# Performance work log

Measured on AMD Instinct MI355X. Metric: run time of the kernel, lower is better.

The kernel has to match this reference:

```python
import jax, jax.numpy as jnp
import numpy as np

D = 1024

def setup_inputs() -> dict:
    key = jax.random.key(0)
    ks = jax.random.split(key, 7)
    s = 1.0 / np.sqrt(D)  # torch Linear default init scale (uniform bound)
    x = jax.random.normal(ks[0], (4, 2048, D), dtype=jnp.float32)
    Wq = jax.random.uniform(ks[1], (D, D), jnp.float32, -s, s)
    Wk = jax.random.uniform(ks[2], (D, D), jnp.float32, -s, s)
    Wv = jax.random.uniform(ks[3], (D, D), jnp.float32, -s, s)
    bq = jax.random.uniform(ks[4], (D,), jnp.float32, -s, s)
    bk = jax.random.uniform(ks[5], (D,), jnp.float32, -s, s)
    bv = jax.random.uniform(ks[6], (D,), jnp.float32, -s, s)
    return {"x": x, "Wq": Wq, "bq": bq, "Wk": Wk, "bk": bk, "Wv": Wv, "bv": bv}

def reference(x, Wq, bq, Wk, bk, Wv, bv):
    # Linear layers: y = x @ W^T + b (weights stored torch-style [out, in])
    Q = jnp.einsum('bsd,ed->bse', x, Wq) + bq
    K = jnp.einsum('bsd,ed->bse', x, Wk) + bk
    V = jnp.einsum('bsd,ed->bse', x, Wv) + bv
    scale = jnp.sqrt(jnp.asarray(Q.shape[-1], Q.dtype))
    scores = jnp.einsum('bqd,bkd->bqk', Q, K) / scale  # [B, S, S]
    probs = jax.nn.softmax(scores, axis=-1)
    return jnp.einsum('bqk,bkd->bqd', probs, V)
```

## Files before the change

kernel.cpp:

```cpp
#include <hip/hip_runtime.h>


typedef __bf16 bf16x8 __attribute__((ext_vector_type(8)));
typedef float f32x4 __attribute__((ext_vector_type(4)));
typedef unsigned short u16;

__device__ __forceinline__ u16 f2b(float f) {
  union { float f; unsigned u; } a; a.f = f;
  unsigned r = a.u + 0x7fffu + ((a.u >> 16) & 1u);
  return (u16)(r >> 16);
}

__global__ __launch_bounds__(256) void cast_all_kernel(const float* __restrict__ x,
                                                       const float* __restrict__ Wq,
                                                       const float* __restrict__ Wk,
                                                       const float* __restrict__ Wv,
                                                       u16* __restrict__ xb,
                                                       u16* __restrict__ Wb) {
  int b = blockIdx.x;
  if (b < 8192) {
    const int i = b * 256 + threadIdx.x;
    float4 v = reinterpret_cast<const float4*>(x)[i];
    reinterpret_cast<ushort4*>(xb)[i] =
        make_ushort4(f2b(v.x), f2b(v.y), f2b(v.z), f2b(v.w));
  } else {
    b -= 8192;
    const int w = b >> 10;
    const float* src = (w == 0) ? Wq : (w == 1) ? Wk : Wv;
    const int i = (b & 1023) * 256 + threadIdx.x;
    float4 v = reinterpret_cast<const float4*>(src)[i];
    reinterpret_cast<ushort4*>(Wb + (size_t)w * 1048576)[i] =
        make_ushort4(f2b(v.x), f2b(v.y), f2b(v.z), f2b(v.w));
  }
}

template <int GEOM, int NT>
__device__ __forceinline__ void core2(const char* __restrict__ Ab,
                                      const char* __restrict__ Bb, int lda, int ldb,
                                      char* smem, f32x4* acc) {
  constexpr int LDSBUF = GEOM ? 49152 : 65536;
  constexpr int BOFF = GEOM ? 16384 : 32768;
  constexpr int AHALF = GEOM ? 8192 : 16384;
  constexpr int NA = GEOM ? 4 : 8;
  const int tid = threadIdx.x;
  const int wave = tid >> 6, lane = tid & 63;
  const int wr = wave >> 2, wc = wave & 3;
  const int fr = lane & 15, fg = lane >> 4;
  const int rd = (fr * 64 + fg * 16) ^ (((fr >> 3) & 1) << 5);
  const int li = (lane * 16) ^ ((lane >> 5) << 5);
  const int sr = li >> 6, sc2 = li & 63;

  auto STAGE = [&](int kt, int s) {
    char* base = smem + (kt & 1) * LDSBUF;
    const int colOff = kt * 128 + s * 64 + sc2;
    char* ldsA = base + s * AHALF;
    __builtin_amdgcn_global_load_lds(
        (const __attribute__((address_space(1))) void*)(Ab + (size_t)(wave * 16 + sr) * lda + colOff),
        (__attribute__((address_space(3))) void*)(ldsA + wave * 1024), 16, 0, 0);
    if constexpr (GEOM == 0)
      __builtin_amdgcn_global_load_lds(
          (const __attribute__((address_space(1))) void*)(Ab + (size_t)((8 + wave) * 16 + sr) * lda + colOff),
          (__attribute__((address_space(3))) void*)(ldsA + 8192 + wave * 1024), 16, 0, 0);
    char* ldsB = base + BOFF + s * 16384;
    __builtin_amdgcn_global_load_lds(
        (const __attribute__((address_space(1))) void*)(Bb + (size_t)(wave * 16 + sr) * ldb + colOff),
        (__attribute__((address_space(3))) void*)(ldsB + wave * 1024), 16, 0, 0);
    __builtin_amdgcn_global_load_lds(
        (const __attribute__((address_space(1))) void*)(Bb + (size_t)((8 + wave) * 16 + sr) * ldb + colOff),
        (__attribute__((address_space(3))) void*)(ldsB + 8192 + wave * 1024), 16, 0, 0);
  };

  STAGE(0, 0);
  STAGE(0, 1);
  if constexpr (GEOM == 0) asm volatile("s_waitcnt vmcnt(4)" ::: "memory");
  else asm volatile("s_waitcnt vmcnt(3)" ::: "memory");
  __builtin_amdgcn_s_barrier();
  __builtin_amdgcn_sched_barrier(0);

  for (int kt = 0; kt < NT; ++kt) {
    const char* bufA = smem + (kt & 1) * LDSBUF;
    const char* bufB = bufA + BOFF;
#pragma unroll
    for (int s = 0; s < 2; ++s) {
      bf16x8 afr[NA], bfr[4];
#pragma unroll
      for (int m = 0; m < NA; ++m)
        afr[m] = *reinterpret_cast<const bf16x8*>(bufA + s * AHALF + (wr * NA + m) * 1024 + rd);
#pragma unroll
      for (int n = 0; n < 4; ++n)
        bfr[n] = *reinterpret_cast<const bf16x8*>(bufB + s * 16384 + (wc * 4 + n) * 1024 + rd);
      if (kt + 1 < NT) STAGE(kt + 1, s);
      __builtin_amdgcn_s_barrier();
      __builtin_amdgcn_sched_barrier(0);
      __builtin_amdgcn_s_setprio(1);
#pragma unroll
      for (int m = 0; m < NA; ++m)
#pragma unroll
        for (int n = 0; n < 4; ++n)
          acc[m * 4 + n] = __builtin_amdgcn_mfma_f32_16x16x32_bf16(
              afr[m], bfr[n], acc[m * 4 + n], 0, 0, 0);
      __builtin_amdgcn_s_setprio(0);
      if (kt < NT - 1) {
        if constexpr (GEOM == 0) asm volatile("s_waitcnt vmcnt(4)" ::: "memory");
        else asm volatile("s_waitcnt vmcnt(3)" ::: "memory");
      } else if (s == 0) {
        asm volatile("s_waitcnt vmcnt(0)" ::: "memory");
      }
      __builtin_amdgcn_s_barrier();
      __builtin_amdgcn_sched_barrier(0);
    }
  }
}

__global__ __launch_bounds__(512, 2) void proj8_kernel(
    const u16* __restrict__ A, const u16* __restrict__ Bm,
    const float* __restrict__ bq, const float* __restrict__ bk,
    const float* __restrict__ bvv, u16* __restrict__ QK, u16* __restrict__ Vt) {
  extern __shared__ char smem[];
  const int tileM = blockIdx.x * 128, tileN = blockIdx.y * 256;
  f32x4 acc[16] = {};
  core2<1, 16>((const char*)A + (size_t)tileM * 2048,
               (const char*)Bm + (size_t)tileN * 2048, 2048, 2048, smem, acc);
  const int tid = threadIdx.x;
  const int wave = tid >> 6, lane = tid & 63;
  const int wr = wave >> 2, wc = wave & 3, fr = lane & 15, fg = lane >> 4;
  const int w = blockIdx.y >> 2;
  const float* bias = (w == 0) ? bq : (w == 1) ? bk : bvv;
  if (w < 2) {
    u16* O = QK + (size_t)w * 8388608;
#pragma unroll
    for (int mi = 0; mi < 4; ++mi) {
      const int r0 = tileM + wr * 64 + mi * 16 + fg * 4;
#pragma unroll
      for (int n = 0; n < 4; ++n) {
        const int cw = (tileN + wc * 64 + n * 16 + fr) & 1023;
        const float bi = bias[cw];
#pragma unroll
        for (int jj = 0; jj < 4; ++jj)
          O[(size_t)(r0 + jj) * 1024 + cw] = f2b(acc[mi * 4 + n][jj] + bi);
      }
    }
  } else {
#pragma unroll
    for (int mi = 0; mi < 4; ++mi) {
      const int r0 = tileM + wr * 64 + mi * 16 + fg * 4;
      const int b = r0 >> 11, s0 = r0 & 2047;
#pragma unroll
      for (int n = 0; n < 4; ++n) {
        const int cw = (tileN + wc * 64 + n * 16 + fr) & 1023;
        const float bi = bias[cw];
        ushort4 u = make_ushort4(f2b(acc[mi * 4 + n][0] + bi), f2b(acc[mi * 4 + n][1] + bi),
                                 f2b(acc[mi * 4 + n][2] + bi), f2b(acc[mi * 4 + n][3] + bi));
        *reinterpret_cast<ushort4*>(&Vt[(size_t)b * 2097152 + (size_t)cw * 2048 + s0]) = u;
      }
    }
  }
}

__global__ __launch_bounds__(512, 2) void sc8_kernel(const u16* __restrict__ Qb,
                                                     const u16* __restrict__ Kb,
                                                     u16* __restrict__ P,
                                                     float* __restrict__ rowpart) {
  extern __shared__ char smem[];
  const int z = blockIdx.z;
  const int tileM = blockIdx.x * 256, tileN = blockIdx.y * 256;
  f32x4 acc[32] = {};
  core2<0, 16>((const char*)Qb + (size_t)z * 4194304 + (size_t)tileM * 2048,
               (const char*)Kb + (size_t)z * 4194304 + (size_t)tileN * 2048, 2048, 2048,
               smem, acc);
  const int tid = threadIdx.x;
  const int wave = tid >> 6, lane = tid & 63;
  const int wr = wave >> 2, wc = wave & 3, fr = lane & 15, fg = lane >> 4;
  float* rs = (float*)smem;
  u16* Po = P + (size_t)z * 4194304 + (size_t)tileM * 2048 + tileN;
#pragma unroll
  for (int mi = 0; mi < 8; ++mi) {
#pragma unroll
    for (int jj = 0; jj < 4; ++jj) {
      const int rl = wr * 128 + mi * 16 + fg * 4 + jj;
      float part = 0.f;
#pragma unroll
      for (int n = 0; n < 4; ++n) {
        float e = __expf(acc[mi * 4 + n][jj] * 0.03125f);
        part += e;
        Po[(size_t)rl * 2048 + wc * 64 + n * 16 + fr] = f2b(e);
      }
      part += __shfl_xor(part, 1);
      part += __shfl_xor(part, 2);
      part += __shfl_xor(part, 4);
      part += __shfl_xor(part, 8);
      if (fr == 0) rs[wc * 256 + rl] = part;
    }
  }
  __syncthreads();
  if (tid < 256) {
    float s = rs[tid] + rs[256 + tid] + rs[512 + tid] + rs[768 + tid];
    rowpart[(size_t)blockIdx.y * 8192 + z * 2048 + tileM + tid] = s;
  }
}

__global__ __launch_bounds__(512, 2) void pv8_kernel(const u16* __restrict__ P,
                                                     const u16* __restrict__ Vt,
                                                     const float* __restrict__ rowpart,
                                                     float* __restrict__ out) {
  extern __shared__ char smem[];
  const int z = blockIdx.z;
  const int tileM = blockIdx.x * 128, tileN = blockIdx.y * 256;
  float* rinv = (float*)(smem + 98304);
  const int tid = threadIdx.x;
  if (tid < 128) {
    float s = 0.f;
#pragma unroll
    for (int t = 0; t < 8; ++t) s += rowpart[t * 8192 + z * 2048 + tileM + tid];
    rinv[tid] = 1.0f / s;
  }
  __builtin_amdgcn_sched_barrier(0);
  f32x4 acc[16] = {};
  core2<1, 32>((const char*)P + (size_t)z * 8388608 + (size_t)tileM * 4096,
               (const char*)Vt + (size_t)z * 4194304 + (size_t)tileN * 4096, 4096, 4096,
               smem, acc);
  const int wave = tid >> 6, lane = tid & 63;
  const int wr = wave >> 2, wc = wave & 3, fr = lane & 15, fg = lane >> 4;
  float* O = out + (size_t)z * 2097152;
#pragma unroll
  for (int mi = 0; mi < 4; ++mi) {
#pragma unroll
    for (int jj = 0; jj < 4; ++jj) {
      const int r = wr * 64 + mi * 16 + fg * 4 + jj;
      const float inv = rinv[r];
#pragma unroll
      for (int n = 0; n < 4; ++n)
        O[(size_t)(tileM + r) * 1024 + tileN + wc * 64 + n * 16 + fr] =
            acc[mi * 4 + n][jj] * inv;
    }
  }
}

extern "C" void kernel_launch(void* const* d_in, const int* in_sizes, int n_in,
                              void* d_out, int out_size, void* d_ws, size_t ws_size,
                              hipStream_t stream) {
  if (ws_size < ((size_t)72 << 20)) return;
  const float* x = (const float*)d_in[0];
  const float* Wq = (const float*)d_in[1];
  const float* bq = (const float*)d_in[2];
  const float* Wk = (const float*)d_in[3];
  const float* bk = (const float*)d_in[4];
  const float* Wv = (const float*)d_in[5];
  const float* bv = (const float*)d_in[6];
  char* ws = (char*)d_ws;
  u16* xb = (u16*)(ws);
  u16* Pb = (u16*)(ws);
  u16* Qb = (u16*)(ws + ((size_t)16 << 20));
  u16* Kb = (u16*)(ws + ((size_t)32 << 20));
  u16* Vt = (u16*)(ws + ((size_t)48 << 20));
  u16* Wb = (u16*)(ws + ((size_t)64 << 20));
  float* rowpart = (float*)(ws + ((size_t)70 << 20));
  float* out = (float*)d_out;

  (void)hipFuncSetAttribute((const void*)proj8_kernel,
                            hipFuncAttributeMaxDynamicSharedMemorySize, 98304);
  (void)hipFuncSetAttribute((const void*)sc8_kernel,
                            hipFuncAttributeMaxDynamicSharedMemorySize, 131072);
  (void)hipFuncSetAttribute((const void*)pv8_kernel,
                            hipFuncAttributeMaxDynamicSharedMemorySize, 98816);

  cast_all_kernel<<<11264, 256, 0, stream>>>(x, Wq, Wk, Wv, xb, Wb);

  proj8_kernel<<<dim3(64, 12), 512, 98304, stream>>>(xb, Wb, bq, bk, bv, Qb, Vt);

  sc8_kernel<<<dim3(8, 8, 4), 512, 131072, stream>>>(Qb, Kb, Pb, rowpart);
  pv8_kernel<<<dim3(16, 4, 4), 512, 98816, stream>>>(Pb, Vt, rowpart, out);
}
```

Before: 155.5 us.

## Software-pipeline GEMM core: prefetch LDS fragments before MFMAs and deepen staging

Restructures the shared GEMM main loop used by all three matmul kernels. It issues one extra half-stage of global-to-LDS loads ahead, and loads the next sub-step's A/B fragments from LDS into a second register set while the MFMAs of the current sub-step run. Both changes aim to hide LDS read latency and global load latency behind MFMA work. In exchange it uses more registers for the double fragment buffers, which could add spills or lower occupancy, and its waitcnt and barrier choreography is more intricate and easier to get wrong.

```diff
diff --git a/kernel.cpp b/kernel.cpp
--- a/kernel.cpp
+++ b/kernel.cpp
@@ -34,10 +34,12 @@
   }
 }
 
+#define VMCNT(n) asm volatile("s_waitcnt vmcnt(" #n ")" ::: "memory")
+
 template <int GEOM, int NT>
-__device__ __forceinline__ void core2(const char* __restrict__ Ab,
-                                      const char* __restrict__ Bb, int lda, int ldb,
-                                      char* smem, f32x4* acc) {
+__device__ __forceinline__ void core2p(const char* __restrict__ Ab,
+                                       const char* __restrict__ Bb, int lda, int ldb,
+                                       char* smem, f32x4* acc) {
   constexpr int LDSBUF = GEOM ? 49152 : 65536;
   constexpr int BOFF = GEOM ? 16384 : 32768;
   constexpr int AHALF = GEOM ? 8192 : 16384;
@@ -69,46 +71,67 @@
         (const __attribute__((address_space(1))) void*)(Bb + (size_t)((8 + wave) * 16 + sr) * ldb + colOff),
         (__attribute__((address_space(3))) void*)(ldsB + 8192 + wave * 1024), 16, 0, 0);
   };
+  auto RD_A = [&](const char* buf, int s, bf16x8* a) {
+#pragma unroll
+    for (int m = 0; m < NA; ++m)
+      a[m] = *reinterpret_cast<const bf16x8*>(buf + s * AHALF + (wr * NA + m) * 1024 + rd);
+  };
+  auto RD_B = [&](const char* buf, int s, bf16x8* b) {
+#pragma unroll
+    for (int n = 0; n < 4; ++n)
+      b[n] = *reinterpret_cast<const bf16x8*>(buf + BOFF + s * 16384 + (wc * 4 + n) * 1024 + rd);
+  };
+  auto MFMA = [&](bf16x8* a, bf16x8* b) {
+    __builtin_amdgcn_s_setprio(1);
+#pragma unroll
+    for (int m = 0; m < NA; ++m)
+#pragma unroll
+      for (int n = 0; n < 4; ++n)
+        acc[m * 4 + n] = __builtin_amdgcn_mfma_f32_16x16x32_bf16(a[m], b[n], acc[m * 4 + n], 0, 0, 0);
+    __builtin_amdgcn_s_setprio(0);
+  };
 
   STAGE(0, 0);
   STAGE(0, 1);
-  if constexpr (GEOM == 0) asm volatile("s_waitcnt vmcnt(4)" ::: "memory");
-  else asm volatile("s_waitcnt vmcnt(3)" ::: "memory");
+  STAGE(1, 0);
+  if constexpr (GEOM == 0) VMCNT(8); else VMCNT(6);
   __builtin_amdgcn_s_barrier();
   __builtin_amdgcn_sched_barrier(0);
 
+  bf16x8 a0[NA], a1[NA], b0[4], b1[4];
+  RD_A(smem, 0, a0);
+  if constexpr (GEOM == 1) RD_B(smem, 0, b0);
+
   for (int kt = 0; kt < NT; ++kt) {
-    const char* bufA = smem + (kt & 1) * LDSBUF;
-    const char* bufB = bufA + BOFF;
-#pragma unroll
-    for (int s = 0; s < 2; ++s) {
-      bf16x8 afr[NA], bfr[4];
-#pragma unroll
-      for (int m = 0; m < NA; ++m)
-        afr[m] = *reinterpret_cast<const bf16x8*>(bufA + s * AHALF + (wr * NA + m) * 1024 + rd);
-#pragma unroll
-      for (int n = 0; n < 4; ++n)
-        bfr[n] = *reinterpret_cast<const bf16x8*>(bufB + s * 16384 + (wc * 4 + n) * 1024 + rd);
-      if (kt + 1 < NT) STAGE(kt + 1, s);
+    const char* buf = smem + (kt & 1) * LDSBUF;
+    const char* bufN = smem + ((kt + 1) & 1) * LDSBUF;
+    if (kt + 1 < NT) STAGE(kt + 1, 1);
+    if (kt < NT - 1) { if constexpr (GEOM == 0) VMCNT(8); else VMCNT(6); }
+    else VMCNT(0);
+    __builtin_amdgcn_s_barrier();
+    if constexpr (GEOM == 0) RD_B(buf, 0, b0);
+    RD_A(buf, 1, a1);
+    if constexpr (GEOM == 1) RD_B(buf, 1, b1);
+    __builtin_amdgcn_sched_barrier(0);
+    MFMA(a0, b0);
+    __builtin_amdgcn_s_barrier();
+    if (kt + 2 < NT) STAGE(kt + 2, 0);
+    if (kt < NT - 1) {
+      if (kt < NT - 2) { if constexpr (GEOM == 0) VMCNT(8); else VMCNT(6); }
+      else             { if constexpr (GEOM == 0) VMCNT(4); else VMCNT(3); }
       __builtin_amdgcn_s_barrier();
+      if constexpr (GEOM == 0) RD_B(buf, 1, b1);
+      RD_A(bufN, 0, a0);
+      if constexpr (GEOM == 1) RD_B(bufN, 0, b0);
       __builtin_amdgcn_sched_barrier(0);
-      __builtin_amdgcn_s_setprio(1);
-#pragma unroll
-      for (int m = 0; m < NA; ++m)
-#pragma unroll
-        for (int n = 0; n < 4; ++n)
-          acc[m * 4 + n] = __builtin_amdgcn_mfma_f32_16x16x32_bf16(
-              afr[m], bfr[n], acc[m * 4 + n], 0, 0, 0);
-      __builtin_amdgcn_s_setprio(0);
-      if (kt < NT - 1) {
-        if constexpr (GEOM == 0) asm volatile("s_waitcnt vmcnt(4)" ::: "memory");
-        else asm volatile("s_waitcnt vmcnt(3)" ::: "memory");
-      } else if (s == 0) {
-        asm volatile("s_waitcnt vmcnt(0)" ::: "memory");
-      }
+      MFMA(a1, b1);
+    } else {
       __builtin_amdgcn_s_barrier();
+      if constexpr (GEOM == 0) RD_B(buf, 1, b1);
       __builtin_amdgcn_sched_barrier(0);
-    }
+      MFMA(a1, b1);
+    }
+    __builtin_amdgcn_s_barrier();
   }
 }
 
@@ -119,8 +142,8 @@
   extern __shared__ char smem[];
   const int tileM = blockIdx.x * 128, tileN = blockIdx.y * 256;
   f32x4 acc[16] = {};
-  core2<1, 16>((const char*)A + (size_t)tileM * 2048,
-               (const char*)Bm + (size_t)tileN * 2048, 2048, 2048, smem, acc);
+  core2p<1, 16>((const char*)A + (size_t)tileM * 2048,
+                (const char*)Bm + (size_t)tileN * 2048, 2048, 2048, smem, acc);
   const int tid = threadIdx.x;
   const int wave = tid >> 6, lane = tid & 63;
   const int wr = wave >> 2, wc = wave & 3, fr = lane & 15, fg = lane >> 4;
@@ -165,9 +188,9 @@
   const int z = blockIdx.z;
   const int tileM = blockIdx.x * 256, tileN = blockIdx.y * 256;
   f32x4 acc[32] = {};
-  core2<0, 16>((const char*)Qb + (size_t)z * 4194304 + (size_t)tileM * 2048,
-               (const char*)Kb + (size_t)z * 4194304 + (size_t)tileN * 2048, 2048, 2048,
-               smem, acc);
+  core2p<0, 16>((const char*)Qb + (size_t)z * 4194304 + (size_t)tileM * 2048,
+                (const char*)Kb + (size_t)z * 4194304 + (size_t)tileN * 2048, 2048, 2048,
+                smem, acc);
   const int tid = threadIdx.x;
   const int wave = tid >> 6, lane = tid & 63;
   const int wr = wave >> 2, wc = wave & 3, fr = lane & 15, fg = lane >> 4;
@@ -216,9 +239,9 @@
   }
   __builtin_amdgcn_sched_barrier(0);
   f32x4 acc[16] = {};
-  core2<1, 32>((const char*)P + (size_t)z * 8388608 + (size_t)tileM * 4096,
-               (const char*)Vt + (size_t)z * 4194304 + (size_t)tileN * 4096, 4096, 4096,
-               smem, acc);
+  core2p<1, 32>((const char*)P + (size_t)z * 8388608 + (size_t)tileM * 4096,
+                (const char*)Vt + (size_t)z * 4194304 + (size_t)tileN * 4096, 4096, 4096,
+                smem, acc);
   const int wave = tid >> 6, lane = tid & 63;
   const int wr = wave >> 2, wc = wave & 3, fr = lane & 15, fg = lane >> 4;
   float* O = out + (size_t)z * 2097152;
```

Result: no change. 157.1 us (+1.1%).
